# Performance work log

Hardware: AMD Instinct MI355X
Metric: run time of the kernel (lower is better)

## Reference

```python
import jax, jax.numpy as jnp
import numpy as np
import math

D_MODEL = 1024
NUM_HEADS = 16
DIM_FF = 4096
B, N = 4, 1024
GRID = 32
R_LEFT = 1.0
R_RIGHT = 1.0
LN_EPS = 1e-5


def get_alibi_slopes(n_heads):
    def pow2(n):
        start = 2 ** (-2 ** (-(math.log2(n) - 3)))
        return [start * start ** i for i in range(n)]
    if math.log2(n_heads).is_integer():
        slopes = pow2(n_heads)
    else:
        m = 2 ** math.floor(math.log2(n_heads))
        slopes = pow2(m)
        slopes += [slopes[-1] * 0.5 ** (i + 1) for i in range(n_heads - m)]
    return jnp.asarray(np.array(slopes, dtype=np.float32))


def setup_inputs() -> dict:
    key = jax.random.key(0)
    ks = jax.random.split(key, 16)
    s = 1.0 / math.sqrt(D_MODEL)
    inp = {
        "src": jax.random.normal(ks[0], (B, N, D_MODEL), jnp.float32),
        "coords": jax.random.randint(ks[1], (B, N, 2), 0, GRID, jnp.int32),
        "Wq": jax.random.normal(ks[2], (D_MODEL, D_MODEL), jnp.float32) * s,
        "Wk": jax.random.normal(ks[3], (D_MODEL, D_MODEL), jnp.float32) * s,
        "Wv": jax.random.normal(ks[4], (D_MODEL, D_MODEL), jnp.float32) * s,
        "Wo": jax.random.normal(ks[5], (D_MODEL, D_MODEL), jnp.float32) * s,
        "W1": jax.random.normal(ks[6], (DIM_FF, D_MODEL), jnp.float32) * s,
        "b1": jnp.zeros((DIM_FF,), jnp.float32),
        "W2": jax.random.normal(ks[7], (D_MODEL, DIM_FF), jnp.float32) * (1.0 / math.sqrt(DIM_FF)),
        "b2": jnp.zeros((D_MODEL,), jnp.float32),
        "g1": jnp.ones((D_MODEL,), jnp.float32),
        "be1": jnp.zeros((D_MODEL,), jnp.float32),
        "g2": jnp.ones((D_MODEL,), jnp.float32),
        "be2": jnp.zeros((D_MODEL,), jnp.float32),
    }
    return inp


def layer_norm(x, g, b):
    mu = jnp.mean(x, axis=-1, keepdims=True)
    var = jnp.mean(jnp.square(x - mu), axis=-1, keepdims=True)
    return (x - mu) * jax.lax.rsqrt(var + LN_EPS) * g + b


def alibi_2d_bias(coords, slopes):
    # coords: (B, N, 2) int -> bias (B, H, N, N)
    x = coords[..., 0].astype(jnp.float32)
    y = coords[..., 1].astype(jnp.float32)
    dist = jnp.abs(x[:, :, None] - x[:, None, :]) + jnp.abs(y[:, :, None] - y[:, None, :])
    flat = y * (x.max() + 1.0) + x  # global x.max(), matching torch code
    le = (flat[:, None, :] <= flat[:, :, None]).astype(jnp.float32)  # (B,N,N)
    s = slopes.reshape(1, -1, 1, 1)
    left = s * R_LEFT
    right = s * R_RIGHT
    return dist[:, None] * (le[:, None] * left + (1.0 - le[:, None]) * right)


def reference(src, coords, Wq, Wk, Wv, Wo, W1, b1, W2, b2, g1, be1, g2, be2):
    H, Hd = NUM_HEADS, D_MODEL // NUM_HEADS
    scale = Hd ** (-0.5)
    slopes = get_alibi_slopes(H)
    bias = alibi_2d_bias(coords, slopes)  # (B,H,N,N)

    Bn, Nn, D = src.shape
    q = (src @ Wq.T).reshape(Bn, Nn, H, Hd)
    k = (src @ Wk.T).reshape(Bn, Nn, H, Hd)
    v = (src @ Wv.T).reshape(Bn, Nn, H, Hd)
    attn = jnp.einsum("bnhd,bmhd->bhnm", q, k) * scale + bias
    attn = jax.nn.softmax(attn, axis=-1)
    out = jnp.einsum("bhnm,bmhd->bnhd", attn, v).reshape(Bn, Nn, D)
    src2 = out @ Wo.T

    x = layer_norm(src + src2, g1, be1)
    ff = (jax.nn.gelu(x @ W1.T + b1, approximate=False)) @ W2.T + b2
    return layer_norm(x + ff, g2, be2)
```

## Files before the change

kernel.cpp:

```cpp
#include <hip/hip_runtime.h>
#include <hip/hip_bf16.h>
#include <math.h>

#define DEV __device__ __forceinline__

typedef __attribute__((ext_vector_type(4))) float f32x4;
typedef __attribute__((ext_vector_type(16))) float f32x16;
typedef __attribute__((ext_vector_type(8))) short bf16x8;
typedef __attribute__((ext_vector_type(4))) unsigned short us4;

DEV unsigned short f2bf(float f) {
    union { float f; unsigned u; } v; v.f = f;
    unsigned r = v.u + 0x7FFF + ((v.u >> 16) & 1);
    return (unsigned short)(r >> 16);
}

DEV void async16(const void* g, void* l) {
    __builtin_amdgcn_global_load_lds(
        (const __attribute__((address_space(1))) void*)g,
        (__attribute__((address_space(3))) void*)l, 16, 0, 0);
}

__global__ void cvt_kernel(const float* __restrict__ in, unsigned short* __restrict__ out, int n4) {
    int i = blockIdx.x * blockDim.x + threadIdx.x;
    if (i >= n4) return;
    f32x4 v = ((const f32x4*)in)[i];
    us4 o;
    o.x = f2bf(v.x); o.y = f2bf(v.y); o.z = f2bf(v.z); o.w = f2bf(v.w);
    ((us4*)out)[i] = o;
}

#define BM 128
#define BN 128
#define BKK 64

template<int EPI>
__global__ __launch_bounds__(256) void gemm_bt(
    const unsigned short* __restrict__ A,
    const unsigned short* __restrict__ B,
    float* __restrict__ Cf, unsigned short* __restrict__ Cb,
    const float* __restrict__ bias,
    int M, int N, int K)
{
    __shared__ unsigned short As[BM * BKK];
    __shared__ unsigned short Bs[BN * BKK];

    const int tid  = threadIdx.x;
    const int wid  = tid >> 6, lane = tid & 63;
    const int l15  = lane & 15, l16 = lane >> 4;
    const int wr   = wid >> 1, wc = wid & 1;
    const int row0 = blockIdx.y * BM;
    const int col0 = blockIdx.x * BN;

    f32x4 acc[4][4] = {};

    const int nkt = K / BKK;
    for (int kt = 0; kt < nkt; ++kt) {
        const int k0 = kt * BKK;
        __syncthreads();
#pragma unroll
        for (int i = 0; i < 4; ++i) {
            int c = i * 256 + tid;
            int row = c >> 3, slot = c & 7;
            int ks = (slot ^ (row & 7)) * 8;
            async16(A + (size_t)(row0 + row) * K + k0 + ks, (char*)As + c * 16);
            async16(B + (size_t)(col0 + row) * K + k0 + ks, (char*)Bs + c * 16);
        }
        __syncthreads();
#pragma unroll
        for (int kk = 0; kk < 2; ++kk) {
            bf16x8 af[4], bfr[4];
#pragma unroll
            for (int m = 0; m < 4; ++m) {
                int r = wr * 64 + m * 16 + l15;
                int slot = (kk * 4 + l16) ^ (r & 7);
                af[m] = *(const bf16x8*)((const char*)As + r * 128 + slot * 16);
            }
#pragma unroll
            for (int n = 0; n < 4; ++n) {
                int r = wc * 64 + n * 16 + l15;
                int slot = (kk * 4 + l16) ^ (r & 7);
                bfr[n] = *(const bf16x8*)((const char*)Bs + r * 128 + slot * 16);
            }
#pragma unroll
            for (int m = 0; m < 4; ++m)
#pragma unroll
                for (int n = 0; n < 4; ++n)
                    acc[m][n] = __builtin_amdgcn_mfma_f32_16x16x32_bf16(af[m], bfr[n], acc[m][n], 0, 0, 0);
        }
    }

#pragma unroll
    for (int m = 0; m < 4; ++m) {
        int grow = row0 + wr * 64 + m * 16 + l16 * 4;
#pragma unroll
        for (int n = 0; n < 4; ++n) {
            int gcol = col0 + wc * 64 + n * 16 + l15;
            float bv = (EPI >= 2) ? bias[gcol] : 0.f;
#pragma unroll
            for (int r = 0; r < 4; ++r) {
                float v = acc[m][n][r];
                size_t idx = (size_t)(grow + r) * N + gcol;
                if (EPI == 0) {
                    Cb[idx] = f2bf(v);
                } else if (EPI == 1) {
                    Cf[idx] = v;
                } else if (EPI == 2) {
                    v += bv;
                    v = 0.5f * v * (1.f + erff(v * 0.70710678118f));
                    Cb[idx] = f2bf(v);
                } else {
                    Cf[idx] = v + bv;
                }
            }
        }
    }
}

__global__ __launch_bounds__(256) void transpose_v(const unsigned short* __restrict__ qkv,
                                                   unsigned short* __restrict__ vt)
{
    __shared__ unsigned short t[64][72];
    const int n0 = blockIdx.x * 64;
    const int bh = blockIdx.y;
    const int b = bh >> 4, h = bh & 15;
    const int tid = threadIdx.x;
#pragma unroll
    for (int i = 0; i < 2; ++i) {
        int c = i * 256 + tid;
        int row = c >> 3, col0 = (c & 7) * 8;
        const unsigned short* src = qkv + (size_t)(b * 1024 + n0 + row) * 3072 + 2048 + h * 64 + col0;
        bf16x8 v = *(const bf16x8*)src;
#pragma unroll
        for (int j = 0; j < 8; ++j) t[row][col0 + j] = (unsigned short)v[j];
    }
    __syncthreads();
#pragma unroll
    for (int i = 0; i < 2; ++i) {
        int c = i * 256 + tid;
        int hd = c >> 3, col0 = (c & 7) * 8;
        bf16x8 v;
#pragma unroll
        for (int j = 0; j < 8; ++j) v[j] = (short)t[col0 + j][hd];
        *(bf16x8*)(vt + ((size_t)bh * 64 + hd) * 1024 + n0 + col0) = v;
    }
}

__global__ __launch_bounds__(256) void attn_kernel(const unsigned short* __restrict__ qkv,
                                                   const int* __restrict__ coords,
                                                   const unsigned short* __restrict__ vt,
                                                   unsigned short* __restrict__ out)
{
    __shared__ unsigned short Ks[2][64 * 64];
    __shared__ unsigned short Vs[2][64 * 64];
    __shared__ float cF[1024 * 2];

    const int tid = threadIdx.x, wid = tid >> 6, lane = tid & 63;
    const int l31 = lane & 31, hi = lane >> 5;
    const int q0 = blockIdx.x * 128;
    const int bh = blockIdx.y;
    const int b = bh >> 4, h = bh & 15;
    const float LOG2E = 1.4426950408889634f;
    const float slope2 = exp2f(-0.5f * (float)(h + 1)) * LOG2E;
    const float scale2 = 0.125f * LOG2E;

    const int c0 = tid,       r0c = c0 >> 3, ks0 = ((c0 & 7) ^ (r0c & 7)) * 8;
    const int c1 = 256 + tid, r1c = c1 >> 3, ks1 = ((c1 & 7) ^ (r1c & 7)) * 8;
    const unsigned short* kbase = qkv + (size_t)(b * 1024) * 3072 + 1024 + h * 64;
    const unsigned short* vbase = vt + (size_t)bh * 64 * 1024;

    {
        const int2* cp = (const int2*)coords + b * 1024;
#pragma unroll
        for (int i = 0; i < 4; ++i) {
            int kv = i * 256 + tid;
            int2 c = cp[kv];
            cF[kv * 2]     = slope2 * (float)c.x;
            cF[kv * 2 + 1] = slope2 * (float)c.y;
        }
    }

    const int qrow = q0 + wid * 32 + l31;
    bf16x8 qf[4];
    {
        const unsigned short* qp = qkv + (size_t)(b * 1024 + qrow) * 3072 + h * 64 + hi * 8;
        qf[0] = *(const bf16x8*)qp;
        qf[1] = *(const bf16x8*)(qp + 16);
        qf[2] = *(const bf16x8*)(qp + 32);
        qf[3] = *(const bf16x8*)(qp + 48);
    }
    float qxs, qys;
    {
        int2 qc = ((const int2*)coords)[b * 1024 + qrow];
        qxs = slope2 * (float)qc.x; qys = slope2 * (float)qc.y;
    }

    float mr = -1e30f, lr = 0.f;
    f32x16 o0 = (f32x16)0.f, o1 = (f32x16)0.f;

    async16(kbase + (size_t)r0c * 3072 + ks0, (char*)Ks[0] + c0 * 16);
    async16(kbase + (size_t)r1c * 3072 + ks1, (char*)Ks[0] + c1 * 16);
    async16(vbase + (size_t)r0c * 1024 + ks0, (char*)Vs[0] + c0 * 16);
    async16(vbase + (size_t)r1c * 1024 + ks1, (char*)Vs[0] + c1 * 16);
    int cur = 0;

    for (int t = 0; t < 16; ++t) {
        const int kv0 = t * 64;
        __syncthreads();
        if (t < 15) {
            const int kv1 = kv0 + 64;
            async16(kbase + (size_t)(kv1 + r0c) * 3072 + ks0, (char*)Ks[cur ^ 1] + c0 * 16);
            async16(kbase + (size_t)(kv1 + r1c) * 3072 + ks1, (char*)Ks[cur ^ 1] + c1 * 16);
            async16(vbase + (size_t)r0c * 1024 + kv1 + ks0, (char*)Vs[cur ^ 1] + c0 * 16);
            async16(vbase + (size_t)r1c * 1024 + kv1 + ks1, (char*)Vs[cur ^ 1] + c1 * 16);
        }

        f32x16 s0 = (f32x16)0.f, s1 = (f32x16)0.f;
        __builtin_amdgcn_s_setprio(1);
#pragma unroll
        for (int c16 = 0; c16 < 4; ++c16) {
            int slot = ((c16 * 2 + hi) ^ (l31 & 7)) * 16;
            bf16x8 k0f = *(const bf16x8*)((const char*)Ks[cur] + l31 * 128 + slot);
            bf16x8 k1f = *(const bf16x8*)((const char*)Ks[cur] + (32 + l31) * 128 + slot);
            s0 = __builtin_amdgcn_mfma_f32_32x32x16_bf16(k0f, qf[c16], s0, 0, 0, 0);
            s1 = __builtin_amdgcn_mfma_f32_32x32x16_bf16(k1f, qf[c16], s1, 0, 0, 0);
        }
        __builtin_amdgcn_s_setprio(0);

#pragma unroll
        for (int T = 0; T < 2; ++T) {
            f32x16& S = T ? s1 : s0;
#pragma unroll
            for (int u = 0; u < 4; ++u) {
                int kvb = kv0 + T * 32 + u * 8 + hi * 4;
                f32x4 ca = *(const f32x4*)&cF[kvb * 2];
                f32x4 cb = *(const f32x4*)&cF[kvb * 2 + 4];
                S[4*u+0] = S[4*u+0] * scale2 + (fabsf(qxs - ca.x) + fabsf(qys - ca.y));
                S[4*u+1] = S[4*u+1] * scale2 + (fabsf(qxs - ca.z) + fabsf(qys - ca.w));
                S[4*u+2] = S[4*u+2] * scale2 + (fabsf(qxs - cb.x) + fabsf(qys - cb.y));
                S[4*u+3] = S[4*u+3] * scale2 + (fabsf(qxs - cb.z) + fabsf(qys - cb.w));
            }
        }

        float pm = s0[0];
#pragma unroll
        for (int i = 1; i < 16; ++i) pm = fmaxf(pm, s0[i]);
#pragma unroll
        for (int i = 0; i < 16; ++i) pm = fmaxf(pm, s1[i]);
        pm = fmaxf(pm, __shfl_xor(pm, 32, 64));
        if (__any(pm > mr + 8.0f)) {
            float mn = fmaxf(mr, pm);
            float corr = exp2f(mr - mn);
            mr = mn;
            lr *= corr;
#pragma unroll
            for (int i = 0; i < 16; ++i) { o0[i] *= corr; o1[i] *= corr; }
        }
        float sum = 0.f;
#pragma unroll
        for (int i = 0; i < 16; ++i) { float p = exp2f(s0[i] - mr); s0[i] = p; sum += p; }
#pragma unroll
        for (int i = 0; i < 16; ++i) { float p = exp2f(s1[i] - mr); s1[i] = p; sum += p; }
        sum += __shfl_xor(sum, 32, 64);
        lr += sum;

        bf16x8 pf[4];
#pragma unroll
        for (int c = 0; c < 4; ++c) {
            const f32x16& S = (c < 2) ? s0 : s1;
            const int e = (c & 1) * 8;
            unsigned x0, x1, y0, y1;
            asm("v_cvt_pk_bf16_f32 %0, %1, %2" : "=v"(x0) : "v"(S[e+0]), "v"(S[e+1]));
            asm("v_cvt_pk_bf16_f32 %0, %1, %2" : "=v"(x1) : "v"(S[e+2]), "v"(S[e+3]));
            asm("v_cvt_pk_bf16_f32 %0, %1, %2" : "=v"(y0) : "v"(S[e+4]), "v"(S[e+5]));
            asm("v_cvt_pk_bf16_f32 %0, %1, %2" : "=v"(y1) : "v"(S[e+6]), "v"(S[e+7]));
            asm("v_permlane32_swap_b32 %0, %1" : "+v"(x0), "+v"(y0));
            asm("v_permlane32_swap_b32 %0, %1" : "+v"(x1), "+v"(y1));
            union { unsigned u[4]; bf16x8 v; } pk_;
            pk_.u[0] = x0; pk_.u[1] = x1; pk_.u[2] = y0; pk_.u[3] = y1;
            pf[c] = pk_.v;
        }

        __builtin_amdgcn_s_setprio(1);
#pragma unroll
        for (int c = 0; c < 4; ++c) {
            int slot = ((c * 2 + hi) ^ (l31 & 7)) * 16;
            bf16x8 v0 = *(const bf16x8*)((const char*)Vs[cur] + l31 * 128 + slot);
            bf16x8 v1 = *(const bf16x8*)((const char*)Vs[cur] + (32 + l31) * 128 + slot);
            o0 = __builtin_amdgcn_mfma_f32_32x32x16_bf16(v0, pf[c], o0, 0, 0, 0);
            o1 = __builtin_amdgcn_mfma_f32_32x32x16_bf16(v1, pf[c], o1, 0, 0, 0);
        }
        __builtin_amdgcn_s_setprio(0);
        cur ^= 1;
    }

    const float inv = 1.0f / lr;
    unsigned short* op = out + (size_t)(b * 1024 + qrow) * 1024 + h * 64;
#pragma unroll
    for (int Td = 0; Td < 2; ++Td) {
        const f32x16& O = Td ? o1 : o0;
#pragma unroll
        for (int u = 0; u < 4; ++u) {
            us4 w;
            w.x = f2bf(O[4*u+0] * inv);
            w.y = f2bf(O[4*u+1] * inv);
            w.z = f2bf(O[4*u+2] * inv);
            w.w = f2bf(O[4*u+3] * inv);
            *(us4*)(op + Td * 32 + u * 8 + hi * 4) = w;
        }
    }
}

__global__ __launch_bounds__(256) void ln_kernel(const float* __restrict__ a, const float* __restrict__ bres,
                                                 const float* __restrict__ g, const float* __restrict__ be,
                                                 float* __restrict__ xout, unsigned short* __restrict__ xb)
{
    __shared__ float red[2][4];
    const int row = blockIdx.x, tid = threadIdx.x;
    const int wid = tid >> 6, lane = tid & 63;
    f32x4 v = ((const f32x4*)a)[(size_t)row * 256 + tid] + ((const f32x4*)bres)[(size_t)row * 256 + tid];
    float s1 = v.x + v.y + v.z + v.w;
    float s2 = v.x * v.x + v.y * v.y + v.z * v.z + v.w * v.w;
#pragma unroll
    for (int off = 1; off < 64; off <<= 1) {
        s1 += __shfl_xor(s1, off, 64);
        s2 += __shfl_xor(s2, off, 64);
    }
    if (lane == 0) { red[0][wid] = s1; red[1][wid] = s2; }
    __syncthreads();
    s1 = red[0][0] + red[0][1] + red[0][2] + red[0][3];
    s2 = red[1][0] + red[1][1] + red[1][2] + red[1][3];
    float mu = s1 * (1.f / 1024.f);
    float var = s2 * (1.f / 1024.f) - mu * mu;
    float rstd = rsqrtf(var + 1e-5f);
    f32x4 gv = ((const f32x4*)g)[tid], bev = ((const f32x4*)be)[tid];
    f32x4 y = (v - mu) * rstd * gv + bev;
    if (xout) ((f32x4*)xout)[(size_t)row * 256 + tid] = y;
    if (xb) {
        us4 ob;
        ob.x = f2bf(y.x); ob.y = f2bf(y.y); ob.z = f2bf(y.z); ob.w = f2bf(y.w);
        ((us4*)xb)[(size_t)row * 256 + tid] = ob;
    }
}

extern "C" void kernel_launch(void* const* d_in, const int* in_sizes, int n_in,
                              void* d_out, int out_size, void* d_ws, size_t ws_size,
                              hipStream_t stream) {
    const float* src    = (const float*)d_in[0];
    const int*   coords = (const int*)d_in[1];
    const float* Wq     = (const float*)d_in[2];
    const float* Wk     = (const float*)d_in[3];
    const float* Wv     = (const float*)d_in[4];
    const float* Wo     = (const float*)d_in[5];
    const float* W1     = (const float*)d_in[6];
    const float* b1     = (const float*)d_in[7];
    const float* W2     = (const float*)d_in[8];
    const float* b2     = (const float*)d_in[9];
    const float* g1     = (const float*)d_in[10];
    const float* be1    = (const float*)d_in[11];
    const float* g2     = (const float*)d_in[12];
    const float* be2    = (const float*)d_in[13];
    float* out = (float*)d_out;

    char* ws = (char*)d_ws;
    size_t off = 0;
    auto alloc = [&](size_t bytes) { size_t o = off; off += (bytes + 255) & ~(size_t)255; return o; };

    const size_t BT = 4096;
    size_t qkv_off   = alloc(BT * 3072 * 2);
    size_t attno_off = alloc(BT * 1024 * 2);
    size_t vt_off    = alloc((size_t)64 * 64 * 1024 * 2);
    size_t regionA_end = off;
    size_t x_off    = alloc(BT * 1024 * 4);
    size_t ffs_off  = alloc(BT * 1024 * 4);
    size_t srcb_off = alloc(BT * 1024 * 2);
    size_t wqkv_off = alloc((size_t)3072 * 1024 * 2);
    size_t wo_off   = alloc((size_t)1024 * 1024 * 2);
    size_t w1_off   = alloc((size_t)4096 * 1024 * 2);
    size_t w2_off   = alloc((size_t)1024 * 4096 * 2);
    (void)regionA_end; (void)ws_size; (void)in_sizes; (void)n_in; (void)out_size;

    unsigned short* qkv   = (unsigned short*)(ws + qkv_off);
    unsigned short* attno = (unsigned short*)(ws + attno_off);
    unsigned short* vt    = (unsigned short*)(ws + vt_off);
    float*          x     = (float*)(ws + x_off);
    float*          src2  = (float*)(ws + ffs_off);
    float*          ff    = (float*)(ws + ffs_off);
    unsigned short* srcb  = (unsigned short*)(ws + srcb_off);
    unsigned short* xb    = (unsigned short*)(ws + srcb_off);
    unsigned short* wqkvb = (unsigned short*)(ws + wqkv_off);
    unsigned short* wob   = (unsigned short*)(ws + wo_off);
    unsigned short* w1b   = (unsigned short*)(ws + w1_off);
    unsigned short* w2b   = (unsigned short*)(ws + w2_off);
    unsigned short* h1    = (unsigned short*)(ws + qkv_off);

    auto cvt = [&](const float* in, unsigned short* o, size_t n) {
        int n4 = (int)(n / 4);
        cvt_kernel<<<(n4 + 255) / 256, 256, 0, stream>>>(in, o, n4);
    };
    cvt(src, srcb, BT * 1024);
    cvt(Wq, wqkvb, 1024 * 1024);
    cvt(Wk, wqkvb + 1024 * 1024, 1024 * 1024);
    cvt(Wv, wqkvb + 2 * 1024 * 1024, 1024 * 1024);
    cvt(Wo, wob, 1024 * 1024);
    cvt(W1, w1b, 4096 * 1024);
    cvt(W2, w2b, 1024 * 4096);

    gemm_bt<0><<<dim3(3072 / BN, 4096 / BM), 256, 0, stream>>>(srcb, wqkvb, nullptr, qkv, nullptr, 4096, 3072, 1024);
    transpose_v<<<dim3(16, 64), 256, 0, stream>>>(qkv, vt);
    attn_kernel<<<dim3(8, 64), 256, 0, stream>>>(qkv, coords, vt, attno);
    gemm_bt<1><<<dim3(1024 / BN, 4096 / BM), 256, 0, stream>>>(attno, wob, src2, nullptr, nullptr, 4096, 1024, 1024);
    ln_kernel<<<4096, 256, 0, stream>>>(src, src2, g1, be1, x, xb);
    gemm_bt<2><<<dim3(4096 / BN, 4096 / BM), 256, 0, stream>>>(xb, w1b, nullptr, h1, b1, 4096, 4096, 1024);
    gemm_bt<3><<<dim3(1024 / BN, 4096 / BM), 256, 0, stream>>>(h1, w2b, ff, nullptr, b2, 4096, 1024, 4096);
    ln_kernel<<<4096, 256, 0, stream>>>(x, ff, g2, be2, out, nullptr);
}
```

Baseline: 403.2 us.

## Add double-buffered 256x256 GEMM for FFN1 and XCD-aware block swizzle

Adds a new 512-thread GEMM kernel with 256x256 output tiles and double-buffered LDS staging, where async global-to-LDS loads for the next K tile overlap the MFMA work on the current one. It also raises wave priority around the MFMA block. This kernel replaces the 128x128 GEMM for the W1+GELU projection, the largest GEMM. Both GEMM kernels now remap block indices so consecutive tiles land on the same XCD, to improve L2 locality. The larger tile cuts global reloads per output, at the cost of 128 KB of LDS and high register pressure, and it yields only 256 blocks for that GEMM.

```diff
diff --git a/kernel.cpp b/kernel.cpp
--- a/kernel.cpp
+++ b/kernel.cpp
@@ -19,6 +19,12 @@
     __builtin_amdgcn_global_load_lds(
         (const __attribute__((address_space(1))) void*)g,
         (__attribute__((address_space(3))) void*)l, 16, 0, 0);
+}
+
+DEV int xcd_swizzle(int flat, int nwg) {
+    int q = nwg >> 3, r8 = nwg & 7;
+    int xcd = flat & 7, idx = flat >> 3;
+    return (xcd < r8 ? xcd * (q + 1) : r8 * (q + 1) + (xcd - r8) * q) + idx;
 }
 
 __global__ void cvt_kernel(const float* __restrict__ in, unsigned short* __restrict__ out, int n4) {
@@ -49,8 +55,11 @@
     const int wid  = tid >> 6, lane = tid & 63;
     const int l15  = lane & 15, l16 = lane >> 4;
     const int wr   = wid >> 1, wc = wid & 1;
-    const int row0 = blockIdx.y * BM;
-    const int col0 = blockIdx.x * BN;
+
+    const int nwg  = gridDim.x * gridDim.y;
+    const int flat = xcd_swizzle(blockIdx.y * gridDim.x + blockIdx.x, nwg);
+    const int row0 = (flat / gridDim.x) * BM;
+    const int col0 = (flat % gridDim.x) * BN;
 
     f32x4 acc[4][4] = {};
 
@@ -93,6 +102,99 @@
 #pragma unroll
     for (int m = 0; m < 4; ++m) {
         int grow = row0 + wr * 64 + m * 16 + l16 * 4;
+#pragma unroll
+        for (int n = 0; n < 4; ++n) {
+            int gcol = col0 + wc * 64 + n * 16 + l15;
+            float bv = (EPI >= 2) ? bias[gcol] : 0.f;
+#pragma unroll
+            for (int r = 0; r < 4; ++r) {
+                float v = acc[m][n][r];
+                size_t idx = (size_t)(grow + r) * N + gcol;
+                if (EPI == 0) {
+                    Cb[idx] = f2bf(v);
+                } else if (EPI == 1) {
+                    Cf[idx] = v;
+                } else if (EPI == 2) {
+                    v += bv;
+                    v = 0.5f * v * (1.f + erff(v * 0.70710678118f));
+                    Cb[idx] = f2bf(v);
+                } else {
+                    Cf[idx] = v + bv;
+                }
+            }
+        }
+    }
+}
+
+template<int EPI>
+__global__ __launch_bounds__(512, 2) void gemm256(
+    const unsigned short* __restrict__ A,
+    const unsigned short* __restrict__ B,
+    float* __restrict__ Cf, unsigned short* __restrict__ Cb,
+    const float* __restrict__ bias,
+    int M, int N, int K)
+{
+    __shared__ unsigned short As[2][256 * 64];
+    __shared__ unsigned short Bs[2][256 * 64];
+
+    const int tid = threadIdx.x;
+    const int wid = tid >> 6, lane = tid & 63;
+    const int l15 = lane & 15, l16 = lane >> 4;
+    const int wr = wid >> 2, wc = wid & 3;
+
+    const int nwg  = gridDim.x * gridDim.y;
+    const int flat = xcd_swizzle(blockIdx.y * gridDim.x + blockIdx.x, nwg);
+    const int row0 = (flat / gridDim.x) * 256;
+    const int col0 = (flat % gridDim.x) * 256;
+
+    f32x4 acc[8][4] = {};
+
+    auto stage = [&](int buf, int k0) {
+#pragma unroll
+        for (int i = 0; i < 4; ++i) {
+            int c = i * 512 + tid;
+            int row = c >> 3, slot = c & 7;
+            int ks = (slot ^ (row & 7)) * 8;
+            async16(A + (size_t)(row0 + row) * K + k0 + ks, (char*)As[buf] + c * 16);
+            async16(B + (size_t)(col0 + row) * K + k0 + ks, (char*)Bs[buf] + c * 16);
+        }
+    };
+
+    stage(0, 0);
+    int cur = 0;
+    const int nkt = K / 64;
+    for (int kt = 0; kt < nkt; ++kt) {
+        __syncthreads();
+        if (kt + 1 < nkt) stage(cur ^ 1, (kt + 1) * 64);
+#pragma unroll
+        for (int kk = 0; kk < 2; ++kk) {
+            bf16x8 af[8], bfr[4];
+#pragma unroll
+            for (int m = 0; m < 8; ++m) {
+                int r = wr * 128 + m * 16 + l15;
+                int slot = (kk * 4 + l16) ^ (r & 7);
+                af[m] = *(const bf16x8*)((const char*)As[cur] + r * 128 + slot * 16);
+            }
+#pragma unroll
+            for (int n = 0; n < 4; ++n) {
+                int r = wc * 64 + n * 16 + l15;
+                int slot = (kk * 4 + l16) ^ (r & 7);
+                bfr[n] = *(const bf16x8*)((const char*)Bs[cur] + r * 128 + slot * 16);
+            }
+            __builtin_amdgcn_s_setprio(1);
+#pragma unroll
+            for (int m = 0; m < 8; ++m)
+#pragma unroll
+                for (int n = 0; n < 4; ++n)
+                    acc[m][n] = __builtin_amdgcn_mfma_f32_16x16x32_bf16(af[m], bfr[n], acc[m][n], 0, 0, 0);
+            __builtin_amdgcn_s_setprio(0);
+        }
+        cur ^= 1;
+    }
+
+#pragma unroll
+    for (int m = 0; m < 8; ++m) {
+        int grow = row0 + wr * 128 + m * 16 + l16 * 4;
 #pragma unroll
         for (int n = 0; n < 4; ++n) {
             int gcol = col0 + wc * 64 + n * 16 + l15;
@@ -411,7 +513,7 @@
     attn_kernel<<<dim3(8, 64), 256, 0, stream>>>(qkv, coords, vt, attno);
     gemm_bt<1><<<dim3(1024 / BN, 4096 / BM), 256, 0, stream>>>(attno, wob, src2, nullptr, nullptr, 4096, 1024, 1024);
     ln_kernel<<<4096, 256, 0, stream>>>(src, src2, g1, be1, x, xb);
-    gemm_bt<2><<<dim3(4096 / BN, 4096 / BM), 256, 0, stream>>>(xb, w1b, nullptr, h1, b1, 4096, 4096, 1024);
+    gemm256<2><<<dim3(4096 / 256, 4096 / 256), 512, 0, stream>>>(xb, w1b, nullptr, h1, b1, 4096, 4096, 1024);
     gemm_bt<3><<<dim3(1024 / BN, 4096 / BM), 256, 0, stream>>>(h1, w2b, ff, nullptr, b2, 4096, 1024, 4096);
     ln_kernel<<<4096, 256, 0, stream>>>(x, ff, g2, be2, out, nullptr);
 }
```

Result: no change. 400.2 us (-0.7%).
